# Performance work log

Hardware: AMD Instinct MI355X
Metric: run time of the kernel (lower is better)

## Reference

```python
import jax, jax.numpy as jnp
import numpy as np

# Static dims
N = 512        # nodes
T = 8          # window_size
E = 16384      # edges per timestep
F0, H1, FP = 128, 256, 64   # feat_proj_dims
FN = 16        # noise dim
WIN = FP + FN  # WLE in_channels = 80
WH = 128       # WLE hidden
D_SSM = 1      # TLSSM d_model = d_ssm = 1 (scalar per node pair)
D_STATE = 16
D_CONV = 4
CONV_DIM = D_SSM + 2 * D_STATE          # 33
D_IN = 2 * D_SSM + 2 * D_STATE + 1      # z, xBC, dt -> 35
PRED = 1


def setup_inputs() -> dict:
    key = jax.random.key(0)
    ks = jax.random.split(key, 24)
    s = 0.05
    rn = lambda k, shp: jax.random.normal(k, shp, dtype=jnp.float32) * s
    return {
        "edge_index": jax.random.randint(ks[0], (T, 2, E), 0, N, dtype=jnp.int64),
        "edge_weight": jax.random.uniform(ks[1], (T, E), dtype=jnp.float32),
        "feats": jax.random.normal(ks[2], (T, N, F0), dtype=jnp.float32),
        "noise": jax.random.normal(ks[3], (T, N, FN), dtype=jnp.float32),
        # feat_proj MLP
        "Wp1": rn(ks[4], (F0, H1)), "bp1": jnp.zeros((H1,), jnp.float32),
        "Wp2": rn(ks[5], (H1, FP)), "bp2": jnp.zeros((FP,), jnp.float32),
        # WeightedLinkEncoder
        "wle_W1": rn(ks[6], (WIN, WH)), "wle_b1": jnp.zeros((WH,), jnp.float32),
        "wle_W2": rn(ks[7], (WH, WH)), "wle_b2": jnp.zeros((WH,), jnp.float32),
        "wle_W3": rn(ks[8], (WH, WH)), "wle_b3": jnp.zeros((WH,), jnp.float32),
        "wle_w4": rn(ks[9], (WH, 1)), "wle_b4": jnp.zeros((1,), jnp.float32),
        # TLSSM (Mamba2-style stepwise)
        "W_in": rn(ks[10], (D_SSM, D_IN)),
        "conv_w": rn(ks[11], (CONV_DIM, D_CONV)),
        "conv_b": jnp.zeros((CONV_DIM,), jnp.float32),
        "dt_bias": jnp.zeros((1,), jnp.float32),
        "A_log": jnp.zeros((1,), jnp.float32),
        "D_skip": jnp.ones((1,), jnp.float32) * s,
        "W_out": rn(ks[12], (D_SSM, D_SSM)),
    }


def _forward(edge_index, edge_weight, feats, noise,
             Wp1, bp1, Wp2, bp2,
             wle_W1, wle_b1, wle_W2, wle_b2, wle_W3, wle_b3, wle_w4, wle_b4,
             W_in, conv_w, conv_b, dt_bias, A_log, D_skip, W_out):
    # feat_proj: stacked Linear+ReLU, vectorized over timesteps
    h = jax.nn.relu(feats @ Wp1 + bp1)
    h = jax.nn.relu(h @ Wp2 + bp2)              # [T, N, FP]
    emb = jnp.concatenate([h, noise], axis=-1)

    # WeightedLinkEncoder: node MLP -> weighted sparse propagation -> edge score
    def wle(x, ei, ew):
        hh = jax.nn.relu(x @ wle_W1 + wle_b1)                       # [N, WH]
        msg = ew[:, None] * hh[ei[1]]                               # gather neighbors
        agg = jax.ops.segment_sum(msg, ei[0], num_segments=N)      # scatter-add
        h2 = jax.nn.relu((hh + agg) @ wle_W2 + wle_b2)
        ef = h2[ei[0]] * h2[ei[1]]                                 # per-edge hadamard
        s = jax.nn.relu(ef @ wle_W3 + wle_b3) @ wle_w4 + wle_b4    # [E, 1]
        return s[:, 0]

    scores = jax.vmap(wle)(emb, edge_index, edge_weight)            # [T, E]

    # SparseTensor(...).to_dense(): densify edge scores to N x N per step
    def dens(ei, s):
        return jnp.zeros((N, N), scores.dtype).at[ei[0], ei[1]].set(s)

    dense = jax.vmap(dens)(edge_index, scores).reshape(T, N * N, D_SSM)

    # TLSSM stepwise recurrence over the window, batch = N*N
    A = -jnp.exp(A_log)  # [1]

    def step(carry, xt):
        conv_state, ssm_state = carry                    # [BN,CONV_DIM,D_CONV], [BN,D_SSM,D_STATE]
        zxbcdt = xt @ W_in                               # [BN, D_IN]
        z, xBC, dt = jnp.split(zxbcdt, [D_SSM, D_SSM + CONV_DIM], axis=-1)
        conv_state = jnp.concatenate([conv_state[:, :, 1:], xBC[:, :, None]], axis=-1)
        xBC = jax.nn.silu(jnp.sum(conv_state * conv_w, axis=-1) + conv_b)
        x_, Bm, Cm = jnp.split(xBC, [D_SSM, D_SSM + D_STATE], axis=-1)
        dt = jax.nn.softplus(dt + dt_bias)               # [BN, 1]
        dA = jnp.exp(dt * A)                             # [BN, 1]
        ssm_state = ssm_state * dA[:, :, None] + (dt * x_)[:, :, None] * Bm[:, None, :]
        y = jnp.sum(ssm_state * Cm[:, None, :], axis=-1) + D_skip * x_
        y = y * jax.nn.silu(z)
        return (conv_state, ssm_state), y @ W_out

    conv0 = jnp.zeros((N * N, CONV_DIM, D_CONV), jnp.float32)
    ssm0 = jnp.zeros((N * N, D_SSM, D_STATE), jnp.float32)
    _, ys = jax.lax.scan(step, (conv0, ssm0), dense)     # [T, BN, 1]
    out = ys.reshape(T, N, N)[-PRED:]                    # pred_flag=True: last pred_size steps
    return out


def reference(edge_index, edge_weight, feats, noise,
              Wp1, bp1, Wp2, bp2,
              wle_W1, wle_b1, wle_W2, wle_b2, wle_W3, wle_b3, wle_w4, wle_b4,
              W_in, conv_w, conv_b, dt_bias, A_log, D_skip, W_out):
    return _forward(edge_index, edge_weight, feats, noise,
                    Wp1, bp1, Wp2, bp2,
                    wle_W1, wle_b1, wle_W2, wle_b2, wle_W3, wle_b3, wle_w4, wle_b4,
                    W_in, conv_w, conv_b, dt_bias, A_log, D_skip, W_out)
```

## Files before the change

kernel.cpp:

```cpp
#include <hip/hip_runtime.h>
#include <math.h>

#define Nn 512
#define Tt 8
#define Ee 16384
#define NNc (Nn*Nn)
#define TNr (Tt*Nn)
#define TE  (Tt*Ee)
#define CAP 128

typedef __bf16 bf16x8 __attribute__((ext_vector_type(8)));
typedef float  f32x4  __attribute__((ext_vector_type(4)));
union BU { uint4 q; bf16x8 v; };

__device__ __forceinline__ void dec2(float x0, float x1, unsigned &hi, unsigned &lo){
    unsigned u0 = __float_as_uint(x0), u1 = __float_as_uint(x1);
    unsigned t0 = u0 + 0x7FFFu + ((u0>>16)&1u);
    unsigned t1 = u1 + 0x7FFFu + ((u1>>16)&1u);
    hi = (t0>>16) | (t1 & 0xFFFF0000u);
    float h0 = __uint_as_float(t0 & 0xFFFF0000u);
    float h1 = __uint_as_float(t1 & 0xFFFF0000u);
    float l0 = x0 - h0, l1 = x1 - h1;
    unsigned v0 = __float_as_uint(l0), v1 = __float_as_uint(l1);
    unsigned s0 = v0 + 0x7FFFu + ((v0>>16)&1u);
    unsigned s1 = v1 + 0x7FFFu + ((v1>>16)&1u);
    lo = (s0>>16) | (s1 & 0xFFFF0000u);
}

__device__ __forceinline__ void splitw(float x, unsigned short* ph, unsigned short* pl, int idx){
    unsigned u = __float_as_uint(x);
    unsigned t = u + 0x7FFFu + ((u>>16)&1u);
    ph[idx] = (unsigned short)(t>>16);
    float hf = __uint_as_float(t & 0xFFFF0000u);
    float lf = x - hf;
    unsigned v = __float_as_uint(lf);
    unsigned s = v + 0x7FFFu + ((v>>16)&1u);
    pl[idx] = (unsigned short)(s>>16);
}

#define DECA(Ah, Al, xa, ya) { uint4 hq, lq; \
    dec2(xa.x, xa.y, hq.x, lq.x); \
    dec2(xa.z, xa.w, hq.y, lq.y); \
    dec2(ya.x, ya.y, hq.z, lq.z); \
    dec2(ya.z, ya.w, hq.w, lq.w); \
    Ah.q = hq; Al.q = lq; }

__global__ __launch_bounds__(256) void k_prep(
    const int* __restrict__ ei, const float* __restrict__ W3,
    const float* __restrict__ Wp1, const float* __restrict__ Wp2,
    const float* __restrict__ W1,
    unsigned short* __restrict__ w3h, unsigned short* __restrict__ w3l,
    unsigned short* __restrict__ p1h, unsigned short* __restrict__ p1l,
    unsigned short* __restrict__ p2h, unsigned short* __restrict__ p2l,
    unsigned short* __restrict__ p3h, unsigned short* __restrict__ p3l,
    int* __restrict__ cnt, int* __restrict__ tag, float4* __restrict__ out4)
{
    int tid = threadIdx.x;
    int bid = blockIdx.x;
    if (bid < 64){
        int e = bid*256 + tid;
        int a = ei[7*2*Ee + e], b = ei[7*2*Ee + Ee + e];
        int cell = a*Nn + b;
#pragma unroll
        for (int t=0;t<8;++t) tag[t*NNc + cell] = 0;
        if (e < TNr) cnt[e] = 0;
        float4 z = {0.f,0.f,0.f,0.f};
#pragma unroll
        for (int q=0;q<4;++q) out4[q*16384 + e] = z;
        int i    = e & 7;
        int lane = (e>>3) & 63;
        int jt   = (e>>9) & 7;
        int kt   = e>>12;
        splitw(W3[(kt*32+(lane>>4)*8+i)*128 + jt*16+(lane&15)], w3h, w3l, e);
        return;
    }
    if (bid < 192){
        int idx = (bid-64)*256 + tid;
        int i=idx&7, lane=(idx>>3)&63, jt=(idx>>9)&15, kt=idx>>13;
        splitw(Wp1[(kt*32+(lane>>4)*8+i)*256 + jt*16+(lane&15)], p1h, p1l, idx);
        return;
    }
    if (bid < 256){
        int idx = (bid-192)*256 + tid;
        int i=idx&7, lane=(idx>>3)&63, jt=(idx>>9)&3, kt=idx>>11;
        splitw(Wp2[(kt*32+(lane>>4)*8+i)*64 + jt*16+(lane&15)], p2h, p2l, idx);
        return;
    }
    {
        int idx = (bid-256)*256 + tid;
        int i=idx&7, lane=(idx>>3)&63, jt=(idx>>9)&7, kt=idx>>12;
        int k = kt*32+(lane>>4)*8+i;
        float v = (k < 80) ? W1[k*128 + jt*16+(lane&15)] : 0.f;
        splitw(v, p3h, p3l, idx);
    }
}

__global__ __launch_bounds__(256) void k_mid(
    const int* __restrict__ ei, const float* __restrict__ ew,
    int* __restrict__ cnt, int2* __restrict__ bucket2, int* __restrict__ tag,
    const float* __restrict__ feats, const float* __restrict__ noise,
    const uint4* __restrict__ p1h, const uint4* __restrict__ p1l,
    const float* __restrict__ bp1,
    const uint4* __restrict__ p2h, const uint4* __restrict__ p2l,
    const float* __restrict__ bp2,
    const uint4* __restrict__ p3h, const uint4* __restrict__ p3l,
    const float* __restrict__ b1, float* __restrict__ hh)
{
    __shared__ float h1s[32][260];
    __shared__ float embs[32][100];
    int tid = threadIdx.x;
    if (blockIdx.x >= 128){
        int g = (blockIdx.x - 128)*256 + tid;
        int t = g>>14, e = g&(Ee-1);
        int a = ei[t*2*Ee + e];
        int b = ei[t*2*Ee + Ee + e];
        int cell = t*Nn + a;
        int pos = atomicAdd(&cnt[cell], 1);
        if (pos < CAP) bucket2[(size_t)cell*CAP + pos] = make_int2(b, __float_as_int(ew[g]));
        atomicMax(&tag[t*NNc + a*Nn + b], g+1);
        return;
    }
    int w = tid >> 6, lane = tid & 63;
    int r16 = lane & 15, g4 = lane >> 4;
    int r0 = blockIdx.x*32;
    {
        int row = tid >> 3, c2 = (tid & 7)*2;
        float2 nz = *(const float2*)&noise[(size_t)(r0+row)*16 + c2];
        embs[row][64+c2] = nz.x; embs[row][64+c2+1] = nz.y;
        embs[row][80+c2] = 0.f;  embs[row][80+c2+1] = 0.f;
    }
    const float* __restrict__ pa0 = &feats[(size_t)(r0 + r16)*128];
    const float* __restrict__ pa1 = &feats[(size_t)(r0 + 16 + r16)*128];
    {
        f32x4 a1[4][2];
#pragma unroll
        for (int jl=0;jl<4;++jl){ a1[jl][0]=(f32x4){0,0,0,0}; a1[jl][1]=(f32x4){0,0,0,0}; }
#pragma unroll
        for (int kt=0;kt<4;++kt){
            int k0 = kt*32 + g4*8;
            BU Ah0, Al0, Ah1, Al1;
            { float4 xa=*(const float4*)&pa0[k0], ya=*(const float4*)&pa0[k0+4]; DECA(Ah0,Al0,xa,ya) }
            { float4 xa=*(const float4*)&pa1[k0], ya=*(const float4*)&pa1[k0+4]; DECA(Ah1,Al1,xa,ya) }
#pragma unroll
            for (int jl=0;jl<4;++jl){
                int jt = w*4 + jl;
                BU Bh, Bl;
                Bh.q = p1h[(kt*16+jt)*64 + lane];
                Bl.q = p1l[(kt*16+jt)*64 + lane];
                a1[jl][0] = __builtin_amdgcn_mfma_f32_16x16x32_bf16(Ah0.v, Bh.v, a1[jl][0], 0,0,0);
                a1[jl][0] = __builtin_amdgcn_mfma_f32_16x16x32_bf16(Ah0.v, Bl.v, a1[jl][0], 0,0,0);
                a1[jl][0] = __builtin_amdgcn_mfma_f32_16x16x32_bf16(Al0.v, Bh.v, a1[jl][0], 0,0,0);
                a1[jl][1] = __builtin_amdgcn_mfma_f32_16x16x32_bf16(Ah1.v, Bh.v, a1[jl][1], 0,0,0);
                a1[jl][1] = __builtin_amdgcn_mfma_f32_16x16x32_bf16(Ah1.v, Bl.v, a1[jl][1], 0,0,0);
                a1[jl][1] = __builtin_amdgcn_mfma_f32_16x16x32_bf16(Al1.v, Bh.v, a1[jl][1], 0,0,0);
            }
        }
#pragma unroll
        for (int jl=0;jl<4;++jl){
            int jcol = (w*4+jl)*16 + r16;
            float b = bp1[jcol];
#pragma unroll
            for (int r=0;r<4;++r){
                h1s[g4*4+r][jcol]      = fmaxf(a1[jl][0][r] + b, 0.f);
                h1s[16+g4*4+r][jcol]   = fmaxf(a1[jl][1][r] + b, 0.f);
            }
        }
    }
    __syncthreads();
    {
        f32x4 a2[2];
        a2[0]=(f32x4){0,0,0,0}; a2[1]=(f32x4){0,0,0,0};
#pragma unroll
        for (int kt=0;kt<8;++kt){
            int k0 = kt*32 + g4*8;
            BU Ah0, Al0, Ah1, Al1;
            { float4 xa=*(const float4*)&h1s[r16][k0],    ya=*(const float4*)&h1s[r16][k0+4];    DECA(Ah0,Al0,xa,ya) }
            { float4 xa=*(const float4*)&h1s[16+r16][k0], ya=*(const float4*)&h1s[16+r16][k0+4]; DECA(Ah1,Al1,xa,ya) }
            BU Bh, Bl;
            Bh.q = p2h[(kt*4+w)*64 + lane];
            Bl.q = p2l[(kt*4+w)*64 + lane];
            a2[0] = __builtin_amdgcn_mfma_f32_16x16x32_bf16(Ah0.v, Bh.v, a2[0], 0,0,0);
            a2[0] = __builtin_amdgcn_mfma_f32_16x16x32_bf16(Ah0.v, Bl.v, a2[0], 0,0,0);
            a2[0] = __builtin_amdgcn_mfma_f32_16x16x32_bf16(Al0.v, Bh.v, a2[0], 0,0,0);
            a2[1] = __builtin_amdgcn_mfma_f32_16x16x32_bf16(Ah1.v, Bh.v, a2[1], 0,0,0);
            a2[1] = __builtin_amdgcn_mfma_f32_16x16x32_bf16(Ah1.v, Bl.v, a2[1], 0,0,0);
            a2[1] = __builtin_amdgcn_mfma_f32_16x16x32_bf16(Al1.v, Bh.v, a2[1], 0,0,0);
        }
        int jcol = w*16 + r16;
        float b = bp2[jcol];
#pragma unroll
        for (int r=0;r<4;++r){
            embs[g4*4+r][jcol]    = fmaxf(a2[0][r] + b, 0.f);
            embs[16+g4*4+r][jcol] = fmaxf(a2[1][r] + b, 0.f);
        }
    }
    __syncthreads();
    {
        f32x4 a3[2][2];
#pragma unroll
        for (int jl=0;jl<2;++jl){ a3[jl][0]=(f32x4){0,0,0,0}; a3[jl][1]=(f32x4){0,0,0,0}; }
#pragma unroll
        for (int kt=0;kt<3;++kt){
            int k0 = kt*32 + g4*8;
            BU Ah0, Al0, Ah1, Al1;
            { float4 xa=*(const float4*)&embs[r16][k0],    ya=*(const float4*)&embs[r16][k0+4];    DECA(Ah0,Al0,xa,ya) }
            { float4 xa=*(const float4*)&embs[16+r16][k0], ya=*(const float4*)&embs[16+r16][k0+4]; DECA(Ah1,Al1,xa,ya) }
#pragma unroll
            for (int jl=0;jl<2;++jl){
                int jt = w*2 + jl;
                BU Bh, Bl;
                Bh.q = p3h[(kt*8+jt)*64 + lane];
                Bl.q = p3l[(kt*8+jt)*64 + lane];
                a3[jl][0] = __builtin_amdgcn_mfma_f32_16x16x32_bf16(Ah0.v, Bh.v, a3[jl][0], 0,0,0);
                a3[jl][0] = __builtin_amdgcn_mfma_f32_16x16x32_bf16(Ah0.v, Bl.v, a3[jl][0], 0,0,0);
                a3[jl][0] = __builtin_amdgcn_mfma_f32_16x16x32_bf16(Al0.v, Bh.v, a3[jl][0], 0,0,0);
                a3[jl][1] = __builtin_amdgcn_mfma_f32_16x16x32_bf16(Ah1.v, Bh.v, a3[jl][1], 0,0,0);
                a3[jl][1] = __builtin_amdgcn_mfma_f32_16x16x32_bf16(Ah1.v, Bl.v, a3[jl][1], 0,0,0);
                a3[jl][1] = __builtin_amdgcn_mfma_f32_16x16x32_bf16(Al1.v, Bh.v, a3[jl][1], 0,0,0);
            }
        }
#pragma unroll
        for (int jl=0;jl<2;++jl){
            int jcol = (w*2+jl)*16 + r16;
            float b = b1[jcol];
#pragma unroll
            for (int r=0;r<4;++r){
                hh[(size_t)(r0+g4*4+r)*128 + jcol]    = fmaxf(a3[jl][0][r] + b, 0.f);
                hh[(size_t)(r0+16+g4*4+r)*128 + jcol] = fmaxf(a3[jl][1][r] + b, 0.f);
            }
        }
    }
}

__global__ __launch_bounds__(256) void k_sw(
    const float* __restrict__ hh, const int* __restrict__ cnt,
    const int2* __restrict__ bucket2,
    const float* __restrict__ W2, const float* __restrict__ b2,
    float* __restrict__ h2)
{
    __shared__ float sx[2][128];
    int dloc = threadIdx.x >> 7;
    int ch = threadIdx.x & 127;
    int bidd = blockIdx.x*2 + dloc;
    int t = bidd >> 9;
    int n = cnt[bidd]; n = n < CAP ? n : CAP;
    const int2* __restrict__ bk = &bucket2[(size_t)bidd*CAP];
    const float* __restrict__ hht = &hh[(size_t)t*Nn*128];
    float acc = hh[(size_t)bidd*128 + ch];
    int i = 0;
    for (; i+1 < n; i += 2){
        int2 p0 = bk[i], p1 = bk[i+1];
        acc += __int_as_float(p0.y)*hht[(size_t)p0.x*128 + ch]
             + __int_as_float(p1.y)*hht[(size_t)p1.x*128 + ch];
    }
    if (i < n){
        int2 p = bk[i];
        acc += __int_as_float(p.y)*hht[(size_t)p.x*128 + ch];
    }
    sx[dloc][ch] = acc;
    __syncthreads();
    float s = 0.f;
    for (int i2=0; i2<128; i2+=4){
        float4 x = *(const float4*)&sx[dloc][i2];
        s += x.x*W2[(i2+0)*128+ch] + x.y*W2[(i2+1)*128+ch]
           + x.z*W2[(i2+2)*128+ch] + x.w*W2[(i2+3)*128+ch];
    }
    h2[(size_t)bidd*128 + ch] = fmaxf(s + b2[ch], 0.f);
}

__global__ __launch_bounds__(512) void k_edge9(
    const int* __restrict__ ei, const float* __restrict__ h2,
    const uint4* __restrict__ w3h, const uint4* __restrict__ w3l,
    const float* __restrict__ b3, const float* __restrict__ w4,
    const float* __restrict__ b4, float* __restrict__ sc)
{
    __shared__ uint4 sBh[2048];
    __shared__ uint4 sBl[2048];
    int tid = threadIdx.x;
    int bid = blockIdx.x;
#pragma unroll
    for (int q=0;q<4;++q){
        sBh[q*512+tid] = w3h[q*512+tid];
        sBl[q*512+tid] = w3l[q*512+tid];
    }
    int tb  = bid >> 6;
    int e0b = (bid & 63) * 256;
    int w   = tid >> 6, lane = tid & 63;
    int e0w = e0b + w*32;
    int r16 = lane & 15, g4 = lane >> 4;

    const int* __restrict__ eit = &ei[tb*2*Ee];
    int a0 = eit[e0w + r16],      s0 = eit[Ee + e0w + r16];
    int a1 = eit[e0w + 16 + r16], s1 = eit[Ee + e0w + 16 + r16];
    const float* __restrict__ pa0 = &h2[(size_t)(tb*Nn+a0)*128];
    const float* __restrict__ pb0 = &h2[(size_t)(tb*Nn+s0)*128];
    const float* __restrict__ pa1 = &h2[(size_t)(tb*Nn+a1)*128];
    const float* __restrict__ pb1 = &h2[(size_t)(tb*Nn+s1)*128];

    f32x4 acc0[8], acc1[8];
#pragma unroll
    for (int jt=0;jt<8;++jt){
        acc0[jt] = (f32x4){0.f,0.f,0.f,0.f};
        acc1[jt] = (f32x4){0.f,0.f,0.f,0.f};
    }

    float4 rA0,rA1,rB0,rB1,rC0,rC1,rD0,rD1;
#define LOADK(kt) { int k0=(kt)*32+g4*8; \
    rA0=*(const float4*)&pa0[k0]; rA1=*(const float4*)&pa0[k0+4]; \
    rB0=*(const float4*)&pb0[k0]; rB1=*(const float4*)&pb0[k0+4]; \
    rC0=*(const float4*)&pa1[k0]; rC1=*(const float4*)&pa1[k0+4]; \
    rD0=*(const float4*)&pb1[k0]; rD1=*(const float4*)&pb1[k0+4]; }

    BU ah0[2], al0[2], ah1[2], al1[2];
#define DECK(s) { uint4 hq,lq; \
    dec2(rA0.x*rB0.x, rA0.y*rB0.y, hq.x, lq.x); \
    dec2(rA0.z*rB0.z, rA0.w*rB0.w, hq.y, lq.y); \
    dec2(rA1.x*rB1.x, rA1.y*rB1.y, hq.z, lq.z); \
    dec2(rA1.z*rB1.z, rA1.w*rB1.w, hq.w, lq.w); \
    ah0[s].q=hq; al0[s].q=lq; \
    dec2(rC0.x*rD0.x, rC0.y*rD0.y, hq.x, lq.x); \
    dec2(rC0.z*rD0.z, rC0.w*rD0.w, hq.y, lq.y); \
    dec2(rC1.x*rD1.x, rC1.y*rD1.y, hq.z, lq.z); \
    dec2(rC1.z*rD1.z, rC1.w*rD1.w, hq.w, lq.w); \
    ah1[s].q=hq; al1[s].q=lq; }

    LOADK(0)
    DECK(0)
    __syncthreads();
#pragma unroll
    for (int kt=0;kt<4;++kt){
        if (kt < 3) LOADK(kt+1)
        const int s = kt & 1;
#pragma unroll
        for (int jt=0;jt<8;++jt){
            BU Bh, Bl;
            Bh.q = sBh[(kt*8+jt)*64 + lane];
            Bl.q = sBl[(kt*8+jt)*64 + lane];
            acc0[jt] = __builtin_amdgcn_mfma_f32_16x16x32_bf16(ah0[s].v, Bh.v, acc0[jt], 0,0,0);
            acc0[jt] = __builtin_amdgcn_mfma_f32_16x16x32_bf16(ah0[s].v, Bl.v, acc0[jt], 0,0,0);
            acc0[jt] = __builtin_amdgcn_mfma_f32_16x16x32_bf16(al0[s].v, Bh.v, acc0[jt], 0,0,0);
            acc1[jt] = __builtin_amdgcn_mfma_f32_16x16x32_bf16(ah1[s].v, Bh.v, acc1[jt], 0,0,0);
            acc1[jt] = __builtin_amdgcn_mfma_f32_16x16x32_bf16(ah1[s].v, Bl.v, acc1[jt], 0,0,0);
            acc1[jt] = __builtin_amdgcn_mfma_f32_16x16x32_bf16(al1[s].v, Bh.v, acc1[jt], 0,0,0);
        }
        if (kt < 3) DECK((kt+1)&1)
    }

    float b4v = b4[0];
    float b3v[8], w4v[8];
#pragma unroll
    for (int jt=0;jt<8;++jt){ b3v[jt] = b3[jt*16 + r16]; w4v[jt] = w4[jt*16 + r16]; }
#pragma unroll
    for (int r=0;r<4;++r){
        float p0 = 0.f, p1 = 0.f;
#pragma unroll
        for (int jt=0;jt<8;++jt){
            p0 += fmaxf(acc0[jt][r] + b3v[jt], 0.f) * w4v[jt];
            p1 += fmaxf(acc1[jt][r] + b3v[jt], 0.f) * w4v[jt];
        }
        p0 += __shfl_xor(p0,1); p0 += __shfl_xor(p0,2);
        p0 += __shfl_xor(p0,4); p0 += __shfl_xor(p0,8);
        p1 += __shfl_xor(p1,1); p1 += __shfl_xor(p1,2);
        p1 += __shfl_xor(p1,4); p1 += __shfl_xor(p1,8);
        if (r16 == 0){
            sc[(size_t)tb*Ee + e0w + g4*4 + r]      = p0 + b4v;
            sc[(size_t)tb*Ee + e0w + 16 + g4*4 + r] = p1 + b4v;
        }
    }
}

__global__ __launch_bounds__(256) void k_ssm2(
    const int* __restrict__ ei, const int* __restrict__ tag,
    const float* __restrict__ sc,
    const float* __restrict__ W_in, const float* __restrict__ conv_w,
    const float* __restrict__ conv_b, const float* __restrict__ dt_bias,
    const float* __restrict__ A_log, const float* __restrict__ D_skip,
    const float* __restrict__ W_out, float* __restrict__ out)
{
    __shared__ float scw[132], scb[33], swin[35];
    int tid = threadIdx.x;
    if (tid < 132) scw[tid] = conv_w[tid];
    if (tid < 33)  scb[tid] = conv_b[tid];
    if (tid < 35)  swin[tid] = W_in[tid];
    __syncthreads();

    int e = blockIdx.x*256 + tid;
    int a = ei[7*2*Ee + e], b = ei[7*2*Ee + Ee + e];
    int cell = a*Nn + b;
    float x[8];
#pragma unroll
    for (int t=0;t<8;++t){
        int tg = tag[t*NNc + cell];
        x[t] = (tg > 0) ? sc[tg-1] : 0.f;
    }

    float A    = -expf(A_log[0]);
    float dtb  = dt_bias[0];
    float dsk  = D_skip[0];
    float wout = W_out[0];
    float win_z = swin[0], win_dt = swin[34];

    float ssm[16];
#pragma unroll
    for (int q=0;q<16;++q) ssm[q]=0.f;
    float h0=0.f,h1=0.f,h2v=0.f;
    float y=0.f;
    for (int t=0;t<8;++t){
        float xt = x[t];
        float act[33];
#pragma unroll
        for (int c=0;c<33;++c){
            float s = h0*scw[c*4+0] + h1*scw[c*4+1] + h2v*scw[c*4+2] + xt*scw[c*4+3];
            float pre = swin[1+c]*s + scb[c];
            act[c] = pre / (1.f + expf(-pre));
        }
        float x_ = act[0];
        float dtr = xt*win_dt + dtb;
        float dt  = (dtr > 20.f) ? dtr : log1pf(expf(dtr));
        float dA  = expf(dt*A);
        float dx  = dt*x_;
        float yv = 0.f;
#pragma unroll
        for (int q=0;q<16;++q){
            ssm[q] = ssm[q]*dA + dx*act[1+q];
            yv += ssm[q]*act[17+q];
        }
        yv += dsk*x_;
        float z = xt*win_z;
        yv *= z / (1.f + expf(-z));
        y = yv;
        h0=h1; h1=h2v; h2v=xt;
    }
    out[cell] = y*wout;
}

extern "C" void kernel_launch(void* const* d_in, const int* in_sizes, int n_in,
                              void* d_out, int out_size, void* d_ws, size_t ws_size,
                              hipStream_t stream)
{
    const int*   ei    = (const int*)d_in[0];
    const float* ew    = (const float*)d_in[1];
    const float* feats = (const float*)d_in[2];
    const float* noise = (const float*)d_in[3];
    const float* Wp1=(const float*)d_in[4];  const float* bp1=(const float*)d_in[5];
    const float* Wp2=(const float*)d_in[6];  const float* bp2=(const float*)d_in[7];
    const float* W1 =(const float*)d_in[8];  const float* b1 =(const float*)d_in[9];
    const float* W2 =(const float*)d_in[10]; const float* b2 =(const float*)d_in[11];
    const float* W3 =(const float*)d_in[12]; const float* b3 =(const float*)d_in[13];
    const float* w4 =(const float*)d_in[14]; const float* b4 =(const float*)d_in[15];
    const float* W_in  =(const float*)d_in[16]; const float* conv_w=(const float*)d_in[17];
    const float* conv_b=(const float*)d_in[18]; const float* dt_bias=(const float*)d_in[19];
    const float* A_log =(const float*)d_in[20]; const float* D_skip=(const float*)d_in[21];
    const float* W_out =(const float*)d_in[22];

    float* out = (float*)d_out;
    float* ws  = (float*)d_ws;
    float* hh    = ws;
    float* h2    = hh    + 524288;
    float* sc    = h2    + 524288;
    int*   cnt   = (int*)(sc + 131072);
    int*   tag   = cnt + TNr;
    int2*  bucket2 = (int2*)(tag + 2097152);
    unsigned short* w3h = (unsigned short*)(bucket2 + (size_t)TNr*CAP);
    unsigned short* w3l = w3h + 16384;
    unsigned short* p1h = w3l + 16384;
    unsigned short* p1l = p1h + 32768;
    unsigned short* p2h = p1l + 32768;
    unsigned short* p2l = p2h + 16384;
    unsigned short* p3h = p2l + 16384;
    unsigned short* p3l = p3h + 12288;

    k_prep <<<304, 256, 0, stream>>>(ei, W3, Wp1, Wp2, W1,
                                     w3h, w3l, p1h, p1l, p2h, p2l, p3h, p3l,
                                     cnt, tag, (float4*)out);
    k_mid  <<<640, 256, 0, stream>>>(ei, ew, cnt, bucket2, tag, feats, noise,
                                     (const uint4*)p1h, (const uint4*)p1l, bp1,
                                     (const uint4*)p2h, (const uint4*)p2l, bp2,
                                     (const uint4*)p3h, (const uint4*)p3l, b1, hh);
    k_sw   <<<TNr/2, 256, 0, stream>>>(hh, cnt, bucket2, W2, b2, h2);
    k_edge9<<<512, 512, 0, stream>>>(ei, h2, (const uint4*)w3h, (const uint4*)w3l,
                                     b3, w4, b4, sc);
    k_ssm2 <<<Ee/256, 256, 0, stream>>>(ei, tag, sc, W_in, conv_w, conv_b,
                                        dt_bias, A_log, D_skip, W_out, out);
}
```

Baseline: 95.58 us.

## Halve edge-kernel block size, drop low-weight LDS copy and register double buffering

The edge scoring kernel now launches twice as many blocks of 256 threads, each covering 128 edges. Only the high-part bf16 W3 matrix is staged in shared memory, and the low part is read straight from global/L2 inside the MFMA loop. The software double buffering of gathered h2 products is removed in favour of loading and decomposing each k-tile just before use. The aim is lower LDS and register pressure so more waves fit per CU, at the cost of exposing global-load latency and repeating W3 staging across more blocks.

```diff
diff --git a/kernel.cpp b/kernel.cpp
--- a/kernel.cpp
+++ b/kernel.cpp
@@ -268,23 +268,19 @@
     h2[(size_t)bidd*128 + ch] = fmaxf(s + b2[ch], 0.f);
 }
 
-__global__ __launch_bounds__(512) void k_edge9(
+__global__ __launch_bounds__(256) void k_edge10(
     const int* __restrict__ ei, const float* __restrict__ h2,
     const uint4* __restrict__ w3h, const uint4* __restrict__ w3l,
     const float* __restrict__ b3, const float* __restrict__ w4,
     const float* __restrict__ b4, float* __restrict__ sc)
 {
     __shared__ uint4 sBh[2048];
-    __shared__ uint4 sBl[2048];
     int tid = threadIdx.x;
     int bid = blockIdx.x;
 #pragma unroll
-    for (int q=0;q<4;++q){
-        sBh[q*512+tid] = w3h[q*512+tid];
-        sBl[q*512+tid] = w3l[q*512+tid];
-    }
-    int tb  = bid >> 6;
-    int e0b = (bid & 63) * 256;
+    for (int q=0;q<8;++q) sBh[q*256+tid] = w3h[q*256+tid];
+    int tb  = bid >> 7;
+    int e0b = (bid & 127) * 128;
     int w   = tid >> 6, lane = tid & 63;
     int e0w = e0b + w*32;
     int r16 = lane & 15, g4 = lane >> 4;
@@ -303,47 +299,44 @@
         acc0[jt] = (f32x4){0.f,0.f,0.f,0.f};
         acc1[jt] = (f32x4){0.f,0.f,0.f,0.f};
     }
-
-    float4 rA0,rA1,rB0,rB1,rC0,rC1,rD0,rD1;
-#define LOADK(kt) { int k0=(kt)*32+g4*8; \
-    rA0=*(const float4*)&pa0[k0]; rA1=*(const float4*)&pa0[k0+4]; \
-    rB0=*(const float4*)&pb0[k0]; rB1=*(const float4*)&pb0[k0+4]; \
-    rC0=*(const float4*)&pa1[k0]; rC1=*(const float4*)&pa1[k0+4]; \
-    rD0=*(const float4*)&pb1[k0]; rD1=*(const float4*)&pb1[k0+4]; }
-
-    BU ah0[2], al0[2], ah1[2], al1[2];
-#define DECK(s) { uint4 hq,lq; \
-    dec2(rA0.x*rB0.x, rA0.y*rB0.y, hq.x, lq.x); \
-    dec2(rA0.z*rB0.z, rA0.w*rB0.w, hq.y, lq.y); \
-    dec2(rA1.x*rB1.x, rA1.y*rB1.y, hq.z, lq.z); \
-    dec2(rA1.z*rB1.z, rA1.w*rB1.w, hq.w, lq.w); \
-    ah0[s].q=hq; al0[s].q=lq; \
-    dec2(rC0.x*rD0.x, rC0.y*rD0.y, hq.x, lq.x); \
-    dec2(rC0.z*rD0.z, rC0.w*rD0.w, hq.y, lq.y); \
-    dec2(rC1.x*rD1.x, rC1.y*rD1.y, hq.z, lq.z); \
-    dec2(rC1.z*rD1.z, rC1.w*rD1.w, hq.w, lq.w); \
-    ah1[s].q=hq; al1[s].q=lq; }
-
-    LOADK(0)
-    DECK(0)
     __syncthreads();
+
 #pragma unroll
     for (int kt=0;kt<4;++kt){
-        if (kt < 3) LOADK(kt+1)
-        const int s = kt & 1;
+        int k0 = kt*32 + g4*8;
+        BU Ah0, Al0, Ah1, Al1;
+        {
+            float4 xa = *(const float4*)&pa0[k0], ya = *(const float4*)&pa0[k0+4];
+            float4 xb = *(const float4*)&pb0[k0], yb = *(const float4*)&pb0[k0+4];
+            uint4 hq, lq;
+            dec2(xa.x*xb.x, xa.y*xb.y, hq.x, lq.x);
+            dec2(xa.z*xb.z, xa.w*xb.w, hq.y, lq.y);
+            dec2(ya.x*yb.x, ya.y*yb.y, hq.z, lq.z);
+            dec2(ya.z*yb.z, ya.w*yb.w, hq.w, lq.w);
+            Ah0.q = hq; Al0.q = lq;
+        }
+        {
+            float4 xa = *(const float4*)&pa1[k0], ya = *(const float4*)&pa1[k0+4];
+            float4 xb = *(const float4*)&pb1[k0], yb = *(const float4*)&pb1[k0+4];
+            uint4 hq, lq;
+            dec2(xa.x*xb.x, xa.y*xb.y, hq.x, lq.x);
+            dec2(xa.z*xb.z, xa.w*xb.w, hq.y, lq.y);
+            dec2(ya.x*yb.x, ya.y*yb.y, hq.z, lq.z);
+            dec2(ya.z*yb.z, ya.w*yb.w, hq.w, lq.w);
+            Ah1.q = hq; Al1.q = lq;
+        }
 #pragma unroll
         for (int jt=0;jt<8;++jt){
             BU Bh, Bl;
             Bh.q = sBh[(kt*8+jt)*64 + lane];
-            Bl.q = sBl[(kt*8+jt)*64 + lane];
-            acc0[jt] = __builtin_amdgcn_mfma_f32_16x16x32_bf16(ah0[s].v, Bh.v, acc0[jt], 0,0,0);
-            acc0[jt] = __builtin_amdgcn_mfma_f32_16x16x32_bf16(ah0[s].v, Bl.v, acc0[jt], 0,0,0);
-            acc0[jt] = __builtin_amdgcn_mfma_f32_16x16x32_bf16(al0[s].v, Bh.v, acc0[jt], 0,0,0);
-            acc1[jt] = __builtin_amdgcn_mfma_f32_16x16x32_bf16(ah1[s].v, Bh.v, acc1[jt], 0,0,0);
-            acc1[jt] = __builtin_amdgcn_mfma_f32_16x16x32_bf16(ah1[s].v, Bl.v, acc1[jt], 0,0,0);
-            acc1[jt] = __builtin_amdgcn_mfma_f32_16x16x32_bf16(al1[s].v, Bh.v, acc1[jt], 0,0,0);
-        }
-        if (kt < 3) DECK((kt+1)&1)
+            Bl.q = w3l[(kt*8+jt)*64 + lane];
+            acc0[jt] = __builtin_amdgcn_mfma_f32_16x16x32_bf16(Ah0.v, Bh.v, acc0[jt], 0,0,0);
+            acc0[jt] = __builtin_amdgcn_mfma_f32_16x16x32_bf16(Ah0.v, Bl.v, acc0[jt], 0,0,0);
+            acc0[jt] = __builtin_amdgcn_mfma_f32_16x16x32_bf16(Al0.v, Bh.v, acc0[jt], 0,0,0);
+            acc1[jt] = __builtin_amdgcn_mfma_f32_16x16x32_bf16(Ah1.v, Bh.v, acc1[jt], 0,0,0);
+            acc1[jt] = __builtin_amdgcn_mfma_f32_16x16x32_bf16(Ah1.v, Bl.v, acc1[jt], 0,0,0);
+            acc1[jt] = __builtin_amdgcn_mfma_f32_16x16x32_bf16(Al1.v, Bh.v, acc1[jt], 0,0,0);
+        }
     }
 
     float b4v = b4[0];
@@ -478,8 +471,8 @@
                                      (const uint4*)p2h, (const uint4*)p2l, bp2,
                                      (const uint4*)p3h, (const uint4*)p3l, b1, hh);
     k_sw   <<<TNr/2, 256, 0, stream>>>(hh, cnt, bucket2, W2, b2, h2);
-    k_edge9<<<512, 512, 0, stream>>>(ei, h2, (const uint4*)w3h, (const uint4*)w3l,
-                                     b3, w4, b4, sc);
+    k_edge10<<<1024, 256, 0, stream>>>(ei, h2, (const uint4*)w3h, (const uint4*)w3l,
+                                       b3, w4, b4, sc);
     k_ssm2 <<<Ee/256, 256, 0, stream>>>(ei, tag, sc, W_in, conv_w, conv_b,
                                         dt_bias, A_log, D_skip, W_out, out);
 }
```

Measured after the change: 101.2 us. 1.06x slower.

## Move k_sw W2 matmul to split-bf16 MFMA with 16 nodes per block

Applied to the files above, without the earlier changes.

The k_sw kernel now processes 16 node-timesteps per 512-thread block. The neighbour aggregation uses float4 loads per thread, and the 128x128 W2 projection runs on bf16 MFMA with a hi/lo split (three products) instead of scalar FMAs. W2 is pre-split and laid out in MFMA fragment order by extra k_prep blocks. This cuts the scalar FMA and global W2 read cost of the dense layer, at the price of extra prep work and a slight precision change from the three-term bf16 emulation.

```diff
diff --git a/kernel.cpp b/kernel.cpp
--- a/kernel.cpp
+++ b/kernel.cpp
@@ -48,11 +48,12 @@
 __global__ __launch_bounds__(256) void k_prep(
     const int* __restrict__ ei, const float* __restrict__ W3,
     const float* __restrict__ Wp1, const float* __restrict__ Wp2,
-    const float* __restrict__ W1,
+    const float* __restrict__ W1, const float* __restrict__ W2,
     unsigned short* __restrict__ w3h, unsigned short* __restrict__ w3l,
     unsigned short* __restrict__ p1h, unsigned short* __restrict__ p1l,
     unsigned short* __restrict__ p2h, unsigned short* __restrict__ p2l,
     unsigned short* __restrict__ p3h, unsigned short* __restrict__ p3l,
+    unsigned short* __restrict__ w2h, unsigned short* __restrict__ w2l,
     int* __restrict__ cnt, int* __restrict__ tag, float4* __restrict__ out4)
 {
     int tid = threadIdx.x;
@@ -86,12 +87,18 @@
         splitw(Wp2[(kt*32+(lane>>4)*8+i)*64 + jt*16+(lane&15)], p2h, p2l, idx);
         return;
     }
-    {
+    if (bid < 304){
         int idx = (bid-256)*256 + tid;
         int i=idx&7, lane=(idx>>3)&63, jt=(idx>>9)&7, kt=idx>>12;
         int k = kt*32+(lane>>4)*8+i;
         float v = (k < 80) ? W1[k*128 + jt*16+(lane&15)] : 0.f;
         splitw(v, p3h, p3l, idx);
+        return;
+    }
+    {
+        int idx = (bid-304)*256 + tid;
+        int i=idx&7, lane=(idx>>3)&63, jt=(idx>>9)&7, kt=idx>>12;
+        splitw(W2[(kt*32+(lane>>4)*8+i)*128 + jt*16+(lane&15)], w2h, w2l, idx);
     }
 }
 
@@ -232,40 +239,64 @@
     }
 }
 
-__global__ __launch_bounds__(256) void k_sw(
+__global__ __launch_bounds__(512) void k_sw2(
     const float* __restrict__ hh, const int* __restrict__ cnt,
     const int2* __restrict__ bucket2,
-    const float* __restrict__ W2, const float* __restrict__ b2,
-    float* __restrict__ h2)
+    const uint4* __restrict__ w2h, const uint4* __restrict__ w2l,
+    const float* __restrict__ b2, float* __restrict__ h2)
 {
-    __shared__ float sx[2][128];
-    int dloc = threadIdx.x >> 7;
-    int ch = threadIdx.x & 127;
-    int bidd = blockIdx.x*2 + dloc;
-    int t = bidd >> 9;
-    int n = cnt[bidd]; n = n < CAP ? n : CAP;
-    const int2* __restrict__ bk = &bucket2[(size_t)bidd*CAP];
-    const float* __restrict__ hht = &hh[(size_t)t*Nn*128];
-    float acc = hh[(size_t)bidd*128 + ch];
-    int i = 0;
-    for (; i+1 < n; i += 2){
-        int2 p0 = bk[i], p1 = bk[i+1];
-        acc += __int_as_float(p0.y)*hht[(size_t)p0.x*128 + ch]
-             + __int_as_float(p1.y)*hht[(size_t)p1.x*128 + ch];
-    }
-    if (i < n){
-        int2 p = bk[i];
-        acc += __int_as_float(p.y)*hht[(size_t)p.x*128 + ch];
-    }
-    sx[dloc][ch] = acc;
+    __shared__ float sx[16][132];
+    int tid = threadIdx.x;
+    int bidd0 = blockIdx.x * 16;
+    {
+        int dloc = tid >> 5;
+        int j4 = tid & 31;
+        int cell = bidd0 + dloc;
+        int t = cell >> 9;
+        int n = cnt[cell]; n = n < CAP ? n : CAP;
+        const int2* __restrict__ bk = &bucket2[(size_t)cell*CAP];
+        const float* __restrict__ hht = &hh[(size_t)t*Nn*128];
+        float4 acc = *(const float4*)&hh[(size_t)cell*128 + j4*4];
+        int i = 0;
+        for (; i+1 < n; i += 2){
+            int2 p0 = bk[i], p1 = bk[i+1];
+            float w0 = __int_as_float(p0.y), w1 = __int_as_float(p1.y);
+            float4 r0 = *(const float4*)&hht[(size_t)p0.x*128 + j4*4];
+            float4 r1 = *(const float4*)&hht[(size_t)p1.x*128 + j4*4];
+            acc.x += w0*r0.x + w1*r1.x;
+            acc.y += w0*r0.y + w1*r1.y;
+            acc.z += w0*r0.z + w1*r1.z;
+            acc.w += w0*r0.w + w1*r1.w;
+        }
+        if (i < n){
+            int2 p = bk[i];
+            float w = __int_as_float(p.y);
+            float4 r = *(const float4*)&hht[(size_t)p.x*128 + j4*4];
+            acc.x += w*r.x; acc.y += w*r.y; acc.z += w*r.z; acc.w += w*r.w;
+        }
+        *(float4*)&sx[dloc][j4*4] = acc;
+    }
     __syncthreads();
-    float s = 0.f;
-    for (int i2=0; i2<128; i2+=4){
-        float4 x = *(const float4*)&sx[dloc][i2];
-        s += x.x*W2[(i2+0)*128+ch] + x.y*W2[(i2+1)*128+ch]
-           + x.z*W2[(i2+2)*128+ch] + x.w*W2[(i2+3)*128+ch];
-    }
-    h2[(size_t)bidd*128 + ch] = fmaxf(s + b2[ch], 0.f);
+    int w = tid >> 6, lane = tid & 63;
+    int r16 = lane & 15, g4 = lane >> 4;
+    f32x4 a = (f32x4){0.f,0.f,0.f,0.f};
+#pragma unroll
+    for (int kt=0;kt<4;++kt){
+        int k0 = kt*32 + g4*8;
+        BU Ah, Al;
+        { float4 xa = *(const float4*)&sx[r16][k0]; float4 ya = *(const float4*)&sx[r16][k0+4]; DECA(Ah,Al,xa,ya) }
+        BU Bh, Bl;
+        Bh.q = w2h[(kt*8+w)*64 + lane];
+        Bl.q = w2l[(kt*8+w)*64 + lane];
+        a = __builtin_amdgcn_mfma_f32_16x16x32_bf16(Ah.v, Bh.v, a, 0,0,0);
+        a = __builtin_amdgcn_mfma_f32_16x16x32_bf16(Ah.v, Bl.v, a, 0,0,0);
+        a = __builtin_amdgcn_mfma_f32_16x16x32_bf16(Al.v, Bh.v, a, 0,0,0);
+    }
+    int jcol = w*16 + r16;
+    float b = b2[jcol];
+#pragma unroll
+    for (int r=0;r<4;++r)
+        h2[(size_t)(bidd0 + g4*4 + r)*128 + jcol] = fmaxf(a[r] + b, 0.f);
 }
 
 __global__ __launch_bounds__(512) void k_edge9(
@@ -469,15 +500,18 @@
     unsigned short* p2l = p2h + 16384;
     unsigned short* p3h = p2l + 16384;
     unsigned short* p3l = p3h + 12288;
-
-    k_prep <<<304, 256, 0, stream>>>(ei, W3, Wp1, Wp2, W1,
+    unsigned short* w2h = p3l + 12288;
+    unsigned short* w2l = w2h + 16384;
+
+    k_prep <<<368, 256, 0, stream>>>(ei, W3, Wp1, Wp2, W1, W2,
                                      w3h, w3l, p1h, p1l, p2h, p2l, p3h, p3l,
-                                     cnt, tag, (float4*)out);
+                                     w2h, w2l, cnt, tag, (float4*)out);
     k_mid  <<<640, 256, 0, stream>>>(ei, ew, cnt, bucket2, tag, feats, noise,
                                      (const uint4*)p1h, (const uint4*)p1l, bp1,
                                      (const uint4*)p2h, (const uint4*)p2l, bp2,
                                      (const uint4*)p3h, (const uint4*)p3l, b1, hh);
-    k_sw   <<<TNr/2, 256, 0, stream>>>(hh, cnt, bucket2, W2, b2, h2);
+    k_sw2  <<<TNr/16, 512, 0, stream>>>(hh, cnt, bucket2,
+                                        (const uint4*)w2h, (const uint4*)w2l, b2, h2);
     k_edge9<<<512, 512, 0, stream>>>(ei, h2, (const uint4*)w3h, (const uint4*)w3l,
                                      b3, w4, b4, sc);
     k_ssm2 <<<Ee/256, 256, 0, stream>>>(ei, tag, sc, W_in, conv_w, conv_b,
```

After: 89.15 us (median of 2 runs). -6.7%, faster.
